# Kernel tuning notes

Hardware: AMD Instinct MI355X
Metric: run time of the kernel (lower is better)

The kernel has to match this reference:

```python
import jax, jax.numpy as jnp
import numpy as np

BN, BE, B = 50000, 800000, 16
NE, EE, GE, EH, NH = 32, 32, 32, 128, 128  # emb dims, hidden dims


def clean(x):
    return jnp.nan_to_num(x, nan=0.0, posinf=0.0, neginf=0.0)


def _lin(key, fan_in, fan_out):
    k1, k2 = jax.random.split(key)
    s = 1.0 / np.sqrt(fan_in)
    return (jax.random.uniform(k1, (fan_in, fan_out), jnp.float32, -s, s),
            jax.random.uniform(k2, (fan_out,), jnp.float32, -s, s))


def setup_inputs() -> dict:
    key = jax.random.key(0)
    ks = jax.random.split(key, 20)
    inp = {
        "x": jax.random.normal(ks[0], (BN, 2), jnp.float32),
        "edge_index": jax.random.randint(ks[1], (2, BE), 0, BN, jnp.int32),
        "batch": jax.random.randint(ks[2], (BN,), 0, B, jnp.int32),
        "node_attr": jnp.ones((BN, 2), jnp.float32),
        "edge_attr": jax.random.uniform(ks[3], (BE, 2), jnp.float32) + 0.5,  # positive spacings
        "glob_attr": jax.random.uniform(ks[4], (B, 2), jnp.float32),
    }
    # encoders (output 2*emb each, 'Duplicated')
    inp["enc_node_W"], inp["enc_node_b"] = _lin(ks[5], 2, 2 * NE)
    inp["enc_edge_W"], inp["enc_edge_b"] = _lin(ks[6], 2, 2 * EE)
    inp["enc_glob_W"], inp["enc_glob_b"] = _lin(ks[7], 2, 2 * GE)
    inp["enc2_W"], inp["enc2_b"] = _lin(ks[8], 2, 2 * EE)
    # derivative MLP: 4*NE+2*EE -> EH -> 2*EE
    inp["dW1"], inp["db1"] = _lin(ks[9], 4 * NE + 2 * EE, EH)
    inp["dW2"], inp["db2"] = _lin(ks[10], EH, 2 * EE)
    # half-jacobian MLP: 4*EE -> EH -> 2*EE
    inp["hW1"], inp["hb1"] = _lin(ks[11], 4 * EE, EH)
    inp["hW2"], inp["hb2"] = _lin(ks[12], EH, 2 * EE)
    # jacobian MLP: 6*EE -> NH -> 2*NE
    inp["jW1"], inp["jb1"] = _lin(ks[13], 6 * EE, NH)
    inp["jW2"], inp["jb2"] = _lin(ks[14], NH, 2 * NE)
    # hessian MLP: 4*EE+2*EE -> NH -> 2*NE
    inp["sW1"], inp["sb1"] = _lin(ks[15], 6 * EE, NH)
    inp["sW2"], inp["sb2"] = _lin(ks[16], NH, 2 * NE)
    # node MLP: 6*NE+2*GE -> NH -> 2*NE
    inp["nW1"], inp["nb1"] = _lin(ks[17], 6 * NE + 2 * GE, NH)
    inp["nW2"], inp["nb2"] = _lin(ks[18], NH, 2 * NE)
    # decoder: 2*NE -> 2
    inp["decW"], inp["decb"] = _lin(ks[19], 2 * NE, 2)
    return inp


def reference(x, edge_index, batch, node_attr, edge_attr, glob_attr,
              enc_node_W, enc_node_b, enc_edge_W, enc_edge_b, enc_glob_W, enc_glob_b,
              enc2_W, enc2_b,
              dW1, db1, dW2, db2,
              hW1, hb1, hW2, hb2,
              jW1, jb1, jW2, jb2,
              sW1, sb1, sW2, sb2,
              nW1, nb1, nW2, nb2,
              decW, decb):
    relu = jax.nn.relu
    seg = lambda d, idx: jax.ops.segment_sum(d, idx, num_segments=BN)
    mlp = lambda t, W1, b1, W2, b2: relu(t @ W1 + b1) @ W2 + b2

    row, col = edge_index[0], edge_index[1]
    spacing = edge_attr                                 # [BE,2]
    inv_spacing = clean(1.0 / spacing)
    inv_double = clean(1.0 / (seg(spacing, row) + seg(spacing, col)))  # [BN,2]

    node_emb = relu(x @ enc_node_W + enc_node_b)        # [BN,2*NE]
    spacing_emb = relu(spacing @ enc_edge_W + enc_edge_b)  # [BE,2*EE]
    glob_emb = relu(glob_attr @ enc_glob_W + enc_glob_b)   # [B,2*GE]
    inv_spacing_emb = relu(inv_spacing @ enc2_W + enc2_b)  # [BE,2*EE]
    inv_double_emb = relu(inv_double @ enc2_W + enc2_b)    # [BN,2*EE]

    d_edge = mlp(jnp.concatenate([node_emb[row], node_emb[col], inv_spacing_emb], -1),
                 dW1, db1, dW2, db2)                    # [BE,2*EE]
    hj_plus = seg(d_edge, row)                          # [BN,2*EE]
    hj_minus = seg(d_edge, col)

    jac1 = seg(mlp(jnp.concatenate([spacing_emb, hj_plus[col]], -1), hW1, hb1, hW2, hb2), col)
    jac2 = seg(mlp(jnp.concatenate([spacing_emb, hj_minus[row]], -1), hW1, hb1, hW2, hb2), row)
    jac = mlp(jnp.concatenate([jac1, jac2, inv_double_emb], -1), jW1, jb1, jW2, jb2)  # [BN,2*NE]

    hess = mlp(jnp.concatenate([hj_plus, hj_minus, inv_double_emb], -1), sW1, sb1, sW2, sb2)

    res = mlp(jnp.concatenate([node_emb, jac, glob_emb[batch], hess], -1), nW1, nb1, nW2, nb2)
    return node_attr * (res @ decW + decb)              # [BN,2]
```

## Files before the change

kernel.cpp:

```cpp
#include <hip/hip_runtime.h>
#include <hip/hip_fp16.h>
#include <math.h>

#define BN 50000
#define BE 800000
#define CHUNK 104
#define NWAVES 7693

typedef _Float16 h2 __attribute__((ext_vector_type(2)));

__device__ __forceinline__ float relu_f(float v) { return fmaxf(v, 0.0f); }
__device__ __forceinline__ float inv_clean(float s) {
    float q = 1.0f / s;
    return isfinite(q) ? q : 0.0f;
}
__device__ __forceinline__ float inv_clean_fast(float s) {
    float q = __builtin_amdgcn_rcpf(s);
    return isfinite(q) ? q : 0.0f;
}
__device__ __forceinline__ float fdot2f(h2 a, h2 b, float c) {
    return __builtin_amdgcn_fdot2(a, b, c, false);
}
__device__ __forceinline__ unsigned int h2u(h2 v) { union { h2 h; unsigned int u; } x; x.h = v; return x.u; }
__device__ __forceinline__ h2 uh2(unsigned int v) { union { unsigned int u; h2 h; } x; x.u = v; return x.h; }
__device__ __forceinline__ unsigned int packh2(float a, float b) {
    h2 h; h.x = (_Float16)a; h.y = (_Float16)b; return h2u(h);
}
__device__ __forceinline__ int pad4(int i) { return i + (i >> 3); }

__global__ __launch_bounds__(256) void k_pack_w1(
    const float* __restrict__ W, int r0, float4* __restrict__ dst)
{
    int t = blockIdx.x * 256 + threadIdx.x;
    if (t >= 2048) return;
    int j2 = t >> 6, l = t & 63;
    const float* ra = W + (size_t)(r0 + 2*j2) * 128 + 2*l;
    const float* rb = W + (size_t)(r0 + 2*j2 + 1) * 128 + 2*l;
    dst[t] = make_float4(ra[0], ra[1], rb[0], rb[1]);
}
__global__ __launch_bounds__(256) void k_pack_uv(
    const float* __restrict__ dW1, float4* __restrict__ dst)
{
    int t = blockIdx.x * 256 + threadIdx.x;
    if (t >= 4096) return;
    int j = t >> 6, l = t & 63;
    float4 w;
    if (l < 32) w = ((const float4*)(dW1 + (size_t)j*128))[l];
    else        w = ((const float4*)(dW1 + (size_t)(64+j)*128))[l-32];
    dst[t] = w;
}
__global__ __launch_bounds__(256) void k_pack_w1h(
    const float* __restrict__ W, int r0, uint2* __restrict__ dst)
{
    int t = blockIdx.x * 256 + threadIdx.x;
    if (t >= 2048) return;
    int j2 = t >> 6, l = t & 63;
    const float* ra = W + (size_t)(r0 + 2*j2) * 128;
    const float* rb = W + (size_t)(r0 + 2*j2 + 1) * 128;
    dst[t] = make_uint2(packh2(ra[2*l],   rb[2*l]),
                        packh2(ra[2*l+1], rb[2*l+1]));
}
__global__ __launch_bounds__(256) void k_pack_w2h(
    const float* __restrict__ W2, uint2* __restrict__ dst)
{
    int t = blockIdx.x * 256 + threadIdx.x;
    if (t >= 2048) return;
    int k4 = t >> 6, l = t & 63;
    dst[t] = make_uint2(packh2(W2[(4*k4+0)*64+l], W2[(4*k4+1)*64+l]),
                        packh2(W2[(4*k4+2)*64+l], W2[(4*k4+3)*64+l]));
}

__global__ __launch_bounds__(256) void k_hist(
    const int* __restrict__ ei, int* __restrict__ rc, int* __restrict__ cc)
{
    int e = blockIdx.x * 256 + threadIdx.x;
    if (e >= BE) return;
    atomicAdd(&rc[ei[e]], 1);
    atomicAdd(&cc[ei[BE + e]], 1);
}

__global__ __launch_bounds__(1024) void k_scan(
    const int* __restrict__ cntR, int* __restrict__ hdR,
    const int* __restrict__ cntC, int* __restrict__ hdC)
{
    __shared__ int s[1024];
    const int* cnt; int* hd;
    if (blockIdx.x == 0) { cnt = cntR; hd = hdR; }
    else                 { cnt = cntC; hd = hdC; }
    int t = threadIdx.x;
    int base = t * 49;
    int sum = 0;
    for (int i = 0; i < 49; i++) {
        int idx = base + i;
        sum += (idx < BN) ? cnt[idx] : 0;
    }
    s[t] = sum;
    __syncthreads();
    for (int o = 1; o < 1024; o <<= 1) {
        int v = (t >= o) ? s[t - o] : 0;
        __syncthreads();
        s[t] += v;
        __syncthreads();
    }
    int run = s[t] - sum;
    for (int i = 0; i < 49; i++) {
        int idx = base + i;
        if (idx < BN) { hd[idx] = run; run += cnt[idx]; }
    }
}

__global__ __launch_bounds__(256) void k_scatter2(
    const int* __restrict__ ei, const float* __restrict__ ea,
    int* __restrict__ rhd, int* __restrict__ chd,
    int4* __restrict__ rs, int4* __restrict__ cs)
{
    int e = blockIdx.x * 256 + threadIdx.x;
    if (e >= BE) return;
    int r = ei[e], c = ei[BE + e];
    float2 s = ((const float2*)ea)[e];
    int s0 = __float_as_int(s.x), s1 = __float_as_int(s.y);
    int p1 = atomicAdd(&rhd[r], 1);
    rs[p1] = make_int4(r, c, s0, s1);
// ... 66 lines not shown
        const int q = l >> 5;
        {
            float2 xa = ((const float2*)x)[n0 + q*4 + 0];
            float2 xb = ((const float2*)x)[n0 + q*4 + 1];
            float2 xc = ((const float2*)x)[n0 + q*4 + 2];
            float2 xd = ((const float2*)x)[n0 + q*4 + 3];
            float4 p0, p1;
            p0.x = relu_f(fmaf(xa.x, w0a, fmaf(xa.y, w0b, b0)));
            p0.y = relu_f(fmaf(xb.x, w0a, fmaf(xb.y, w0b, b0)));
            p0.z = relu_f(fmaf(xc.x, w0a, fmaf(xc.y, w0b, b0)));
            p0.w = relu_f(fmaf(xd.x, w0a, fmaf(xd.y, w0b, b0)));
            p1.x = relu_f(fmaf(xa.x, w1a, fmaf(xa.y, w1b, b1)));
            p1.y = relu_f(fmaf(xb.x, w1a, fmaf(xb.y, w1b, b1)));
            p1.z = relu_f(fmaf(xc.x, w1a, fmaf(xc.y, w1b, b1)));
            p1.w = relu_f(fmaf(xd.x, w1a, fmaf(xd.y, w1b, b1)));
            xb4[jj*2 + q]      = p0;
            xb4[(jj+32)*2 + q] = p1;
        }
        float4 acc[8];
        #pragma unroll
        for (int e = 0; e < 8; e++) acc[e] = make_float4(0,0,0,0);
        #pragma unroll 8
        for (int j = 0; j < 64; j++) {
            float4 wq = guv[j*64 + l];
            float4 xa = xb4[j*2 + 0];
            float4 xc = xb4[j*2 + 1];
            acc[0].x = fmaf(xa.x, wq.x, acc[0].x); acc[0].y = fmaf(xa.x, wq.y, acc[0].y);
            acc[0].z = fmaf(xa.x, wq.z, acc[0].z); acc[0].w = fmaf(xa.x, wq.w, acc[0].w);
            acc[1].x = fmaf(xa.y, wq.x, acc[1].x); acc[1].y = fmaf(xa.y, wq.y, acc[1].y);
            acc[1].z = fmaf(xa.y, wq.z, acc[1].z); acc[1].w = fmaf(xa.y, wq.w, acc[1].w);
            acc[2].x = fmaf(xa.z, wq.x, acc[2].x); acc[2].y = fmaf(xa.z, wq.y, acc[2].y);
            acc[2].z = fmaf(xa.z, wq.z, acc[2].z); acc[2].w = fmaf(xa.z, wq.w, acc[2].w);
            acc[3].x = fmaf(xa.w, wq.x, acc[3].x); acc[3].y = fmaf(xa.w, wq.y, acc[3].y);
            acc[3].z = fmaf(xa.w, wq.z, acc[3].z); acc[3].w = fmaf(xa.w, wq.w, acc[3].w);
            acc[4].x = fmaf(xc.x, wq.x, acc[4].x); acc[4].y = fmaf(xc.x, wq.y, acc[4].y);
            acc[4].z = fmaf(xc.x, wq.z, acc[4].z); acc[4].w = fmaf(xc.x, wq.w, acc[4].w);
            acc[5].x = fmaf(xc.y, wq.x, acc[5].x); acc[5].y = fmaf(xc.y, wq.y, acc[5].y);
            acc[5].z = fmaf(xc.y, wq.z, acc[5].z); acc[5].w = fmaf(xc.y, wq.w, acc[5].w);
            acc[6].x = fmaf(xc.z, wq.x, acc[6].x); acc[6].y = fmaf(xc.z, wq.y, acc[6].y);
            acc[6].z = fmaf(xc.z, wq.z, acc[6].z); acc[6].w = fmaf(xc.z, wq.w, acc[6].w);
            acc[7].x = fmaf(xc.w, wq.x, acc[7].x); acc[7].y = fmaf(xc.w, wq.y, acc[7].y);
            acc[7].z = fmaf(xc.w, wq.z, acc[7].z); acc[7].w = fmaf(xc.w, wq.w, acc[7].w);
        }
        __half* dst = (l < 32) ? (u_h + 4*l) : (v_h + 4*(l-32));
        #pragma unroll
        for (int e = 0; e < 8; e++) {
            __half2* p = (__half2*)(dst + (size_t)(n0+e)*128);
            p[0] = __floats2half2_rn(acc[e].x, acc[e].y);
            p[1] = __floats2half2_rn(acc[e].z, acc[e].w);
        }
    }
}

__global__ __launch_bounds__(256, 4) void k_e1(
    const int4* __restrict__ recs,
    const __half* __restrict__ A_h, const __half* __restrict__ B_h,
    const int* __restrict__ lb, const int* __restrict__ hd, const int* __restrict__ cnt,
    const float* __restrict__ e2w, const float* __restrict__ e2b,
    const uint2* __restrict__ pw1, const float* __restrict__ db1,
    const uint2* __restrict__ pw2, const float* __restrict__ db2,
    float* __restrict__ outAcc)
{
    extern __shared__ unsigned int ldsu[];
    const int wid = threadIdx.x >> 6, l = threadIdx.x & 63;
    uint4* xbuf = (uint4*)ldsu + (size_t)wid * 216;
    uint4* hbuf = xbuf + 72;

    const int wave = blockIdx.x * 4 + wid;
    if (wave >= NWAVES) return;
    const int n0 = lb[wave], n1 = lb[wave + 1];
    if (n0 >= n1) return;
    const int eb = hd[n0] - cnt[n0];
    const int ee = (n1 < BN) ? (hd[n1] - cnt[n1]) : BE;
    if (eb >= ee) return;

    const int j2 = l >> 1, eh = l & 1;
    const float w0a = e2w[2*j2],    w0b = e2w[64+2*j2], eb0 = e2b[2*j2];
    const float w1a = e2w[2*j2+1],  w1b = e2w[65+2*j2], eb1 = e2b[2*j2+1];
    const float b1a = db1[2*l], b1b = db1[2*l+1];
    const float b2r = db2[l];

    float acc = 0.f;
    int cur = -1;

    for (int i = eb; i < ee; i += 8) {
        const int nact = min(8, ee - i);
        int key[8], oth[8];
        float spx[8], spy[8];
        #pragma unroll
        for (int e = 0; e < 8; e++) {
            int idx = i + ((e < nact) ? e : nact - 1);
            int4 rec = recs[idx];
            key[e] = rec.x; oth[e] = rec.y;
            spx[e] = __int_as_float(rec.z); spy[e] = __int_as_float(rec.w);
        }
        {
            uint4 xw;
            unsigned int* xp = (unsigned int*)&xw;
            #pragma unroll
            for (int c = 0; c < 4; c++) {
                int e = 4*eh + c;
                float q0 = inv_clean_fast(spx[e]);
                float q1 = inv_clean_fast(spy[e]);
                float r0 = relu_f(fmaf(q0, w0a, fmaf(q1, w0b, eb0)));
                float r1 = relu_f(fmaf(q0, w1a, fmaf(q1, w1b, eb1)));
                xp[c] = packh2(r0, r1);
            }
            xbuf[pad4(j2*2 + eh)] = xw;
        }
        float t0[8], t1[8];
        #pragma unroll
        for (int e = 0; e < 8; e++) {
            float2 au = __half22float2(*(const __half2*)(A_h + (size_t)key[e]*128 + 2*l));
            float2 bu = __half22float2(*(const __half2*)(B_h + (size_t)oth[e]*128 + 2*l));
            t0[e] = b1a + au.x + bu.x;
            t1[e] = b1b + au.y + bu.y;
        }
        #pragma unroll 8
        for (int p = 0; p < 32; p++) {
            uint4 x0 = xbuf[pad4(p*2 + 0)];
            uint4 x1 = xbuf[pad4(p*2 + 1)];
            uint2 wv = pw1[p*64 + l];
            h2 wa = uh2(wv.x), wb = uh2(wv.y);
            t0[0] = fdot2f(uh2(x0.x), wa, t0[0]); t1[0] = fdot2f(uh2(x0.x), wb, t1[0]);
            t0[1] = fdot2f(uh2(x0.y), wa, t0[1]); t1[1] = fdot2f(uh2(x0.y), wb, t1[1]);
            t0[2] = fdot2f(uh2(x0.z), wa, t0[2]); t1[2] = fdot2f(uh2(x0.z), wb, t1[2]);
            t0[3] = fdot2f(uh2(x0.w), wa, t0[3]); t1[3] = fdot2f(uh2(x0.w), wb, t1[3]);
            t0[4] = fdot2f(uh2(x1.x), wa, t0[4]); t1[4] = fdot2f(uh2(x1.x), wb, t1[4]);
            t0[5] = fdot2f(uh2(x1.y), wa, t0[5]); t1[5] = fdot2f(uh2(x1.y), wb, t1[5]);
            t0[6] = fdot2f(uh2(x1.z), wa, t0[6]); t1[6] = fdot2f(uh2(x1.z), wb, t1[6]);
            t0[7] = fdot2f(uh2(x1.w), wa, t0[7]); t1[7] = fdot2f(uh2(x1.w), wb, t1[7]);
        }
        {
            uint4 hA, hB;
            unsigned int* pa = (unsigned int*)&hA;
            unsigned int* pb = (unsigned int*)&hB;
            #pragma unroll
            for (int c = 0; c < 4; c++) {
                pa[c] = packh2(relu_f(t0[c]),   relu_f(t1[c]));
                pb[c] = packh2(relu_f(t0[4+c]), relu_f(t1[4+c]));
            }
            hbuf[pad4(l*2 + 0)] = hA;
            hbuf[pad4(l*2 + 1)] = hB;
        }
        float o[8] = {0,0,0,0,0,0,0,0};
        #pragma unroll 8
        for (int k4 = 0; k4 < 32; k4++) {
            uint4 a0 = hbuf[pad4(4*k4 + 0)];
            uint4 a1 = hbuf[pad4(4*k4 + 1)];
            uint4 b0 = hbuf[pad4(4*k4 + 2)];
            uint4 b1 = hbuf[pad4(4*k4 + 3)];
            uint2 wv = pw2[k4*64 + l];
            h2 wa = uh2(wv.x), wb = uh2(wv.y);
            o[0] = fdot2f(uh2(b0.x), wb, fdot2f(uh2(a0.x), wa, o[0]));
            o[1] = fdot2f(uh2(b0.y), wb, fdot2f(uh2(a0.y), wa, o[1]));
            o[2] = fdot2f(uh2(b0.z), wb, fdot2f(uh2(a0.z), wa, o[2]));
            o[3] = fdot2f(uh2(b0.w), wb, fdot2f(uh2(a0.w), wa, o[3]));
            o[4] = fdot2f(uh2(b1.x), wb, fdot2f(uh2(a1.x), wa, o[4]));
            o[5] = fdot2f(uh2(b1.y), wb, fdot2f(uh2(a1.y), wa, o[5]));
            o[6] = fdot2f(uh2(b1.z), wb, fdot2f(uh2(a1.z), wa, o[6]));
            o[7] = fdot2f(uh2(b1.w), wb, fdot2f(uh2(a1.w), wa, o[7]));
        }
        #pragma unroll
        for (int e = 0; e < 8; e++) {
            if (e < nact) {
                float val = o[e] + b2r;
                if (key[e] != cur) {
                    if (cur >= 0) outAcc[(size_t)cur*64 + l] = acc;
                    acc = 0.f;
                    cur = key[e];
                }
                acc += val;
            }
        }
    }
    if (cur >= 0) outAcc[(size_t)cur*64 + l] = acc;
}

__global__ __launch_bounds__(256, 6) void k_tptmh(
    const float* __restrict__ hjp, const float* __restrict__ hjm,
    const float4* __restrict__ gtp,
    __half* __restrict__ tp_h, __half* __restrict__ tm_h)
{
    extern __shared__ float lds[];
    const int wid = threadIdx.x >> 6, l = threadIdx.x & 63;
    float4* xb4 = (float4*)(lds + wid * 512);
    const int gw = blockIdx.x * 4 + wid;
    const int nw = gridDim.x * 4;
    const int NG = BN/8;

    for (int vg = gw; vg < 2*NG; vg += nw) {
        const float* in = (vg < NG) ? hjp : hjm;
        __half*     out = (vg < NG) ? tp_h : tm_h;
        const int n0 = ((vg < NG) ? vg : vg - NG) * 8;
        const int q = l >> 5;
        #pragma unroll
        for (int r = 0; r < 2; r++) {
            int j = (l & 31) + 32*r;
            float v0 = in[(n0 + q*4 + 0)*64 + j];
            float v1 = in[(n0 + q*4 + 1)*64 + j];
            float v2 = in[(n0 + q*4 + 2)*64 + j];
            float v3 = in[(n0 + q*4 + 3)*64 + j];
            xb4[j*2 + q] = make_float4(v0, v1, v2, v3);
        }
        float a0[8] = {0,0,0,0,0,0,0,0}, a1[8] = {0,0,0,0,0,0,0,0};
        #pragma unroll 8
        for (int j2 = 0; j2 < 32; j2++) {
            float4 wq = gtp[j2*64 + l];
            float4 xa = xb4[(2*j2)*2 + 0];
            float4 xbv = xb4[(2*j2)*2 + 1];
            float4 xc = xb4[(2*j2+1)*2 + 0];
            float4 xd = xb4[(2*j2+1)*2 + 1];
            a0[0] = fmaf(xa.x, wq.x, fmaf(xc.x, wq.z, a0[0]));
            a1[0] = fmaf(xa.x, wq.y, fmaf(xc.x, wq.w, a1[0]));
            a0[1] = fmaf(xa.y, wq.x, fmaf(xc.y, wq.z, a0[1]));
            a1[1] = fmaf(xa.y, wq.y, fmaf(xc.y, wq.w, a1[1]));
            a0[2] = fmaf(xa.z, wq.x, fmaf(xc.z, wq.z, a0[2]));
            a1[2] = fmaf(xa.z, wq.y, fmaf(xc.z, wq.w, a1[2]));
            a0[3] = fmaf(xa.w, wq.x, fmaf(xc.w, wq.z, a0[3]));
            a1[3] = fmaf(xa.w, wq.y, fmaf(xc.w, wq.w, a1[3]));
            a0[4] = fmaf(xbv.x, wq.x, fmaf(xd.x, wq.z, a0[4]));
            a1[4] = fmaf(xbv.x, wq.y, fmaf(xd.x, wq.w, a1[4]));
            a0[5] = fmaf(xbv.y, wq.x, fmaf(xd.y, wq.z, a0[5]));
            a1[5] = fmaf(xbv.y, wq.y, fmaf(xd.y, wq.w, a1[5]));
            a0[6] = fmaf(xbv.z, wq.x, fmaf(xd.z, wq.z, a0[6]));
            a1[6] = fmaf(xbv.z, wq.y, fmaf(xd.z, wq.w, a1[6]));
            a0[7] = fmaf(xbv.w, wq.x, fmaf(xd.w, wq.z, a0[7]));
            a1[7] = fmaf(xbv.w, wq.y, fmaf(xd.w, wq.w, a1[7]));
        }
        #pragma unroll
        for (int e = 0; e < 8; e++) {
            *(__half2*)(out + (size_t)(n0+e)*128 + 2*l) = __floats2half2_rn(a0[e], a1[e]);
        }
    }
}

__global__ __launch_bounds__(256, 4) void k_e2(
    const int4* __restrict__ recs, const __half* __restrict__ tvals_h,
    const int* __restrict__ lb, const int* __restrict__ hd, const int* __restrict__ cnt,
    const float* __restrict__ eew, const float* __restrict__ eeb,
    const uint2* __restrict__ pw1, const float* __restrict__ hb1,
    const uint2* __restrict__ pw2, const float* __restrict__ hb2,
    float* __restrict__ out)
{
    extern __shared__ unsigned int ldsu[];
    const int wid = threadIdx.x >> 6, l = threadIdx.x & 63;
    uint4* xbuf = (uint4*)ldsu + (size_t)wid * 216;
    uint4* hbuf = xbuf + 72;

    const int wave = blockIdx.x * 4 + wid;
    if (wave >= NWAVES) return;
    const int n0 = lb[wave], n1 = lb[wave + 1];
    if (n0 >= n1) return;
    const int eb = hd[n0] - cnt[n0];
    const int ee = (n1 < BN) ? (hd[n1] - cnt[n1]) : BE;
    if (eb >= ee) return;

    const int j2 = l >> 1, eh = l & 1;
    const float w0a = eew[2*j2],    w0b = eew[64+2*j2], eb0 = eeb[2*j2];
    const float w1a = eew[2*j2+1],  w1b = eew[65+2*j2], eb1 = eeb[2*j2+1];
    const float b1a = hb1[2*l], b1b = hb1[2*l+1];
    const float b2r = hb2[l];

    float acc = 0.f;
    int cur = -1;

    for (int i = eb; i < ee; i += 8) {
        const int nact = min(8, ee - i);
        int key[8];
        float spx[8], spy[8];
        #pragma unroll
        for (int e = 0; e < 8; e++) {
            int idx = i + ((e < nact) ? e : nact - 1);
            int4 rec = recs[idx];
            key[e] = rec.x;
            spx[e] = __int_as_float(rec.z); spy[e] = __int_as_float(rec.w);
        }
        {
            uint4 xw;
            unsigned int* xp = (unsigned int*)&xw;
            #pragma unroll
            for (int c = 0; c < 4; c++) {
                int e = 4*eh + c;
                float r0 = relu_f(fmaf(spx[e], w0a, fmaf(spy[e], w0b, eb0)));
                float r1 = relu_f(fmaf(spx[e], w1a, fmaf(spy[e], w1b, eb1)));
                xp[c] = packh2(r0, r1);
            }
            xbuf[pad4(j2*2 + eh)] = xw;
        }
        float t0[8], t1[8];
        #pragma unroll
        for (int e = 0; e < 8; e++) {
            float2 tv = __half22float2(*(const __half2*)(tvals_h + (size_t)key[e]*128 + 2*l));
            t0[e] = b1a + tv.x;
            t1[e] = b1b + tv.y;
        }
        #pragma unroll 8
        for (int p = 0; p < 32; p++) {
            uint4 x0 = xbuf[pad4(p*2 + 0)];
            uint4 x1 = xbuf[pad4(p*2 + 1)];
            uint2 wv = pw1[p*64 + l];
            h2 wa = uh2(wv.x), wb = uh2(wv.y);
            t0[0] = fdot2f(uh2(x0.x), wa, t0[0]); t1[0] = fdot2f(uh2(x0.x), wb, t1[0]);
            t0[1] = fdot2f(uh2(x0.y), wa, t0[1]); t1[1] = fdot2f(uh2(x0.y), wb, t1[1]);
            t0[2] = fdot2f(uh2(x0.z), wa, t0[2]); t1[2] = fdot2f(uh2(x0.z), wb, t1[2]);
            t0[3] = fdot2f(uh2(x0.w), wa, t0[3]); t1[3] = fdot2f(uh2(x0.w), wb, t1[3]);
            t0[4] = fdot2f(uh2(x1.x), wa, t0[4]); t1[4] = fdot2f(uh2(x1.x), wb, t1[4]);
            t0[5] = fdot2f(uh2(x1.y), wa, t0[5]); t1[5] = fdot2f(uh2(x1.y), wb, t1[5]);
            t0[6] = fdot2f(uh2(x1.z), wa, t0[6]); t1[6] = fdot2f(uh2(x1.z), wb, t1[6]);
            t0[7] = fdot2f(uh2(x1.w), wa, t0[7]); t1[7] = fdot2f(uh2(x1.w), wb, t1[7]);
        }
        {
            uint4 hA, hB;
            unsigned int* pa = (unsigned int*)&hA;
            unsigned int* pb = (unsigned int*)&hB;
            #pragma unroll
            for (int c = 0; c < 4; c++) {
                pa[c] = packh2(relu_f(t0[c]),   relu_f(t1[c]));
                pb[c] = packh2(relu_f(t0[4+c]), relu_f(t1[4+c]));
            }
            hbuf[pad4(l*2 + 0)] = hA;
            hbuf[pad4(l*2 + 1)] = hB;
        }
        float o[8] = {0,0,0,0,0,0,0,0};
        #pragma unroll 8
        for (int k4 = 0; k4 < 32; k4++) {
            uint4 a0 = hbuf[pad4(4*k4 + 0)];
            uint4 a1 = hbuf[pad4(4*k4 + 1)];
            uint4 b0 = hbuf[pad4(4*k4 + 2)];
            uint4 b1 = hbuf[pad4(4*k4 + 3)];
            uint2 wv = pw2[k4*64 + l];
            h2 wa = uh2(wv.x), wb = uh2(wv.y);
            o[0] = fdot2f(uh2(b0.x), wb, fdot2f(uh2(a0.x), wa, o[0]));
            o[1] = fdot2f(uh2(b0.y), wb, fdot2f(uh2(a0.y), wa, o[1]));
            o[2] = fdot2f(uh2(b0.z), wb, fdot2f(uh2(a0.z), wa, o[2]));
            o[3] = fdot2f(uh2(b0.w), wb, fdot2f(uh2(a0.w), wa, o[3]));
            o[4] = fdot2f(uh2(b1.x), wb, fdot2f(uh2(a1.x), wa, o[4]));
            o[5] = fdot2f(uh2(b1.y), wb, fdot2f(uh2(a1.y), wa, o[5]));
            o[6] = fdot2f(uh2(b1.z), wb, fdot2f(uh2(a1.z), wa, o[6]));
            o[7] = fdot2f(uh2(b1.w), wb, fdot2f(uh2(a1.w), wa, o[7]));
        }
        #pragma unroll
        for (int e = 0; e < 8; e++) {
            if (e < nact) {
                float val = o[e] + b2r;
                if (key[e] != cur) {
                    if (cur >= 0) out[(size_t)cur*64 + l] = acc;
                    acc = 0.f;
                    cur = key[e];
                }
                acc += val;
            }
        }
    }
    if (cur >= 0) out[(size_t)cur*64 + l] = acc;
}

__global__ __launch_bounds__(256, 4) void k_node_mlp(
    const float* __restrict__ A, const float* __restrict__ Bv,
    const float* __restrict__ sumsp,
    const float* __restrict__ e2w_g, const float* __restrict__ e2b_g,
    const float* __restrict__ W1g, const float* __restrict__ b1g,
    const float* __restrict__ W2g, const float* __restrict__ b2g,
    float* __restrict__ outp)
{
    extern __shared__ float lds[];
    const int wid = threadIdx.x >> 6, l = threadIdx.x & 63;
    float* xbuf = lds + wid * 768;
    float* hbuf = lds + 4*768 + wid * 512;

    const float ewl = e2w_g[l], ewl2 = e2w_g[64+l], ebl = e2b_g[l];
    const float bb0 = b1g[2*l], bb1 = b1g[2*l+1];
    const float bo = b2g[l];

    const int gw = blockIdx.x * 4 + wid;
    const int nw = gridDim.x * 4;

    for (int g = gw; g < BN/4; g += nw) {
        const int i0 = g * 4;
        float av[4], bv[4], iv[4];
        #pragma unroll
        for (int e = 0; e < 4; e++) {
            int i = i0 + e;
            av[e] = A[i*64 + l];
            bv[e] = Bv[i*64 + l];
            float q0 = inv_clean(sumsp[i*2+0]);
            float q1 = inv_clean(sumsp[i*2+1]);
            iv[e] = relu_f(fmaf(q0, ewl, fmaf(q1, ewl2, ebl)));
        }
        ((float4*)xbuf)[l]       = make_float4(av[0], av[1], av[2], av[3]);
        ((float4*)xbuf)[64 + l]  = make_float4(bv[0], bv[1], bv[2], bv[3]);
        ((float4*)xbuf)[128 + l] = make_float4(iv[0], iv[1], iv[2], iv[3]);

        float acc0[4] = {0,0,0,0}, acc1[4] = {0,0,0,0};
        #pragma unroll 8
        for (int j = 0; j < 192; j++) {
            float4 xv = ((const float4*)xbuf)[j];
            float2 wv = ((const float2*)(W1g + j*128))[l];
            acc0[0] = fmaf(xv.x, wv.x, acc0[0]);
            acc0[1] = fmaf(xv.y, wv.x, acc0[1]);
            acc0[2] = fmaf(xv.z, wv.x, acc0[2]);
            acc0[3] = fmaf(xv.w, wv.x, acc0[3]);
            acc1[0] = fmaf(xv.x, wv.y, acc1[0]);
            acc1[1] = fmaf(xv.y, wv.y, acc1[1]);
            acc1[2] = fmaf(xv.z, wv.y, acc1[2]);
            acc1[3] = fmaf(xv.w, wv.y, acc1[3]);
        }
        #pragma unroll
// ... 101 lines not shown
        }
    }
}

extern "C" void kernel_launch(void* const* d_in, const int* in_sizes, int n_in,
                              void* d_out, int out_size, void* d_ws, size_t ws_size,
                              hipStream_t stream) {
    const float* x          = (const float*)d_in[0];
    const int*   ei         = (const int*)  d_in[1];
    const int*   batch      = (const int*)  d_in[2];
    const float* node_attr  = (const float*)d_in[3];
    const float* edge_attr  = (const float*)d_in[4];
    const float* glob_attr  = (const float*)d_in[5];
    const float* enc_node_W = (const float*)d_in[6];
    const float* enc_node_b = (const float*)d_in[7];
    const float* enc_edge_W = (const float*)d_in[8];
    const float* enc_edge_b = (const float*)d_in[9];
    const float* enc_glob_W = (const float*)d_in[10];
    const float* enc_glob_b = (const float*)d_in[11];
    const float* enc2_W     = (const float*)d_in[12];
    const float* enc2_b     = (const float*)d_in[13];
    const float* dW1 = (const float*)d_in[14]; const float* db1 = (const float*)d_in[15];
    const float* dW2 = (const float*)d_in[16]; const float* db2 = (const float*)d_in[17];
    const float* hW1 = (const float*)d_in[18]; const float* hb1 = (const float*)d_in[19];
    const float* hW2 = (const float*)d_in[20]; const float* hb2 = (const float*)d_in[21];
    const float* jW1 = (const float*)d_in[22]; const float* jb1 = (const float*)d_in[23];
    const float* jW2 = (const float*)d_in[24]; const float* jb2 = (const float*)d_in[25];
    const float* sW1 = (const float*)d_in[26]; const float* sb1 = (const float*)d_in[27];
    const float* sW2 = (const float*)d_in[28]; const float* sb2 = (const float*)d_in[29];
    const float* nW1 = (const float*)d_in[30]; const float* nb1 = (const float*)d_in[31];
    const float* nW2 = (const float*)d_in[32]; const float* nb2 = (const float*)d_in[33];
    const float* decW = (const float*)d_in[34]; const float* decb = (const float*)d_in[35];

    float* ws = (float*)d_ws;
    int4*   rs    = (int4*)ws;
    int4*   cs    = (int4*)(ws + 3200000);
    __half* u_h   = (__half*)(ws + 6400000);
    __half* v_h   = (__half*)(ws + 9600000);
    float*  hjp   = ws + 12800000;
    float*  hjm   = ws + 16000000;
    float*  jac1  = ws + 19200000;
    float*  jac2  = ws + 22400000;
    float*  sumsp = ws + 25600000;
    int*    row_cnt = (int*)(ws + 25700000);
    int*    col_cnt = row_cnt + 50176;
    int*    row_hd  = col_cnt + 50176;
    int*    col_hd  = row_hd + 50048;
    int*    lbr     = col_hd + 50048;
    int*    lbc     = lbr + 7694;

    float* scratch = (float*)d_out;
    float4* puv   = (float4*)(scratch);
    float4* ptp   = (float4*)(scratch + 16384);
    uint2*  pe1w1 = (uint2*)(scratch + 24576);
    uint2*  pe1w2 = (uint2*)(scratch + 28672);
    uint2*  pe2w1 = (uint2*)(scratch + 32768);
    uint2*  pe2w2 = (uint2*)(scratch + 36864);

    hipMemsetAsync(hjp, 0, (size_t)12800000*sizeof(float), stream);
    hipMemsetAsync(row_cnt, 0, (size_t)(2*50176)*sizeof(int), stream);

    k_pack_uv<<<16, 256, 0, stream>>>(dW1, puv);
    k_pack_w1<<<8, 256, 0, stream>>>(hW1, 64, ptp);
    k_pack_w1h<<<8, 256, 0, stream>>>(dW1, 128, pe1w1);
    k_pack_w2h<<<8, 256, 0, stream>>>(dW2, pe1w2);
    k_pack_w1h<<<8, 256, 0, stream>>>(hW1, 0, pe2w1);
    k_pack_w2h<<<8, 256, 0, stream>>>(hW2, pe2w2);

    k_uvh<<<1563, 256, 2048*4, stream>>>(x, enc_node_W, enc_node_b, puv, u_h, v_h);

    k_hist<<<3125, 256, 0, stream>>>(ei, row_cnt, col_cnt);
    k_scan<<<2, 1024, 0, stream>>>(row_cnt, row_hd, col_cnt, col_hd);
    k_scatter2<<<3125, 256, 0, stream>>>(ei, edge_attr, row_hd, col_hd, rs, cs);
    k_sumsp2<<<196, 256, 0, stream>>>(rs, row_hd, row_cnt, cs, col_hd, col_cnt, sumsp);
    k_part<<<61, 256, 0, stream>>>(row_hd, row_cnt, lbr, col_hd, col_cnt, lbc);

    const int E_BLOCKS = (NWAVES + 3) / 4;
    const size_t lds_e = 4 * 216 * 16;

    k_e1<<<E_BLOCKS, 256, lds_e, stream>>>(rs, u_h, v_h, lbr, row_hd, row_cnt,
                                           enc2_W, enc2_b, pe1w1, db1, pe1w2, db2, hjp);
    k_e1<<<E_BLOCKS, 256, lds_e, stream>>>(cs, v_h, u_h, lbc, col_hd, col_cnt,
                                           enc2_W, enc2_b, pe1w1, db1, pe1w2, db2, hjm);

    k_tptmh<<<1536, 256, 2048*4, stream>>>(hjp, hjm, ptp, u_h, v_h);

    k_e2<<<E_BLOCKS, 256, lds_e, stream>>>(cs, u_h, lbc, col_hd, col_cnt,
                                           enc_edge_W, enc_edge_b,
                                           pe2w1, hb1, pe2w2, hb2, jac1);
    k_e2<<<E_BLOCKS, 256, lds_e, stream>>>(rs, v_h, lbr, row_hd, row_cnt,
                                           enc_edge_W, enc_edge_b,
                                           pe2w1, hb1, pe2w2, hb2, jac2);

    size_t lds_nm = (4*768 + 4*512) * sizeof(float);
    k_node_mlp<<<1024, 256, lds_nm, stream>>>(jac1, jac2, sumsp, enc2_W, enc2_b,
                                              jW1, jb1, jW2, jb2, jac1);
    k_node_mlp<<<1024, 256, lds_nm, stream>>>(hjp, hjm, sumsp, enc2_W, enc2_b,
                                              sW1, sb1, sW2, sb2, hjp);

    size_t lds_nf = (4*1024 + 4*512) * sizeof(float);
    k_node_final<<<1024, 256, lds_nf, stream>>>(x, enc_node_W, enc_node_b,
                                                jac1, hjp,
                                                batch, glob_attr, enc_glob_W, enc_glob_b,
                                                nW1, nb1, nW2, nb2, decW, decb,
                                                node_attr, (float*)d_out);
}
```

Baseline: 2.416 ms.

## Replace fdot2 edge-MLP kernels with MFMA 16x16x16 fp16 templated kernel

Rewrites the two per-edge MLP kernels (derivative and half-jacobian) into one templated kernel that processes 16 edges per wave using MFMA 16x16x16 fp16 instructions instead of scalar fdot2 loops through LDS. Weights are repacked into MFMA fragment layout, and the first-layer inputs are built directly in registers. The second-layer output goes through a small LDS tile for the segmented row reduction. This aims to cut the VALU-bound dot-product cost on the 800k-edge passes, at the cost of more per-lane gather granularity and new fragment-layout correctness risk.

After: 2.409 ms. No clear change (-0.3%).

```diff
diff --git a/kernel.cpp b/kernel.cpp
--- a/kernel.cpp
+++ b/kernel.cpp
@@ -8,6 +8,8 @@
 #define NWAVES 7693
 
 typedef _Float16 h2 __attribute__((ext_vector_type(2)));
+typedef _Float16 h4 __attribute__((ext_vector_type(4)));
+typedef float    f4 __attribute__((ext_vector_type(4)));
 
 __device__ __forceinline__ float relu_f(float v) { return fmaxf(v, 0.0f); }
 __device__ __forceinline__ float inv_clean(float s) {
@@ -18,15 +20,12 @@
     float q = __builtin_amdgcn_rcpf(s);
     return isfinite(q) ? q : 0.0f;
 }
-__device__ __forceinline__ float fdot2f(h2 a, h2 b, float c) {
-    return __builtin_amdgcn_fdot2(a, b, c, false);
-}
 __device__ __forceinline__ unsigned int h2u(h2 v) { union { h2 h; unsigned int u; } x; x.h = v; return x.u; }
 __device__ __forceinline__ h2 uh2(unsigned int v) { union { unsigned int u; h2 h; } x; x.u = v; return x.h; }
 __device__ __forceinline__ unsigned int packh2(float a, float b) {
     h2 h; h.x = (_Float16)a; h.y = (_Float16)b; return h2u(h);
 }
-__device__ __forceinline__ int pad4(int i) { return i + (i >> 3); }
+__device__ __forceinline__ h4 u2h4(uint2 v) { union { uint2 u; h4 h; } x; x.u = v; return x.h; }
 
 __global__ __launch_bounds__(256) void k_pack_w1(
     const float* __restrict__ W, int r0, float4* __restrict__ dst)
@@ -49,25 +48,35 @@
     else        w = ((const float4*)(dW1 + (size_t)(64+j)*128))[l-32];
     dst[t] = w;
 }
-__global__ __launch_bounds__(256) void k_pack_w1h(
+__global__ __launch_bounds__(256) void k_pack_a1(
     const float* __restrict__ W, int r0, uint2* __restrict__ dst)
 {
     int t = blockIdx.x * 256 + threadIdx.x;
     if (t >= 2048) return;
-    int j2 = t >> 6, l = t & 63;
-    const float* ra = W + (size_t)(r0 + 2*j2) * 128;
-    const float* rb = W + (size_t)(r0 + 2*j2 + 1) * 128;
-    dst[t] = make_uint2(packh2(ra[2*l],   rb[2*l]),
-                        packh2(ra[2*l+1], rb[2*l+1]));
-}
-__global__ __launch_bounds__(256) void k_pack_w2h(
+    int frag = t >> 6, l = t & 63;
+    int n = frag >> 2, s = frag & 3;
+    int i = l & 15, kq = l >> 4;
+    size_t base = (size_t)(r0 + s*16 + kq*4) * 128 + n*16 + i;
+    float w0 = W[base + 0*128];
+    float w1 = W[base + 1*128];
+    float w2 = W[base + 2*128];
+    float w3 = W[base + 3*128];
+    dst[t] = make_uint2(packh2(w0, w1), packh2(w2, w3));
+}
+__global__ __launch_bounds__(256) void k_pack_a2(
     const float* __restrict__ W2, uint2* __restrict__ dst)
 {
     int t = blockIdx.x * 256 + threadIdx.x;
     if (t >= 2048) return;
-    int k4 = t >> 6, l = t & 63;
-    dst[t] = make_uint2(packh2(W2[(4*k4+0)*64+l], W2[(4*k4+1)*64+l]),
-                        packh2(W2[(4*k4+2)*64+l], W2[(4*k4+3)*64+l]));
+    int frag = t >> 6, l = t & 63;
+    int m = frag >> 3, n = frag & 7;
+    int i = l & 15, kq = l >> 4;
+    size_t base = (size_t)(n*16 + kq*4) * 64 + m*16 + i;
+    float w0 = W2[base + 0*64];
+    float w1 = W2[base + 1*64];
+    float w2 = W2[base + 2*64];
+    float w3 = W2[base + 3*64];
+    dst[t] = make_uint2(packh2(w0, w1), packh2(w2, w3));
 }
 
 __global__ __launch_bounds__(256) void k_hist(
@@ -240,129 +249,115 @@
     }
 }
 
-__global__ __launch_bounds__(256, 4) void k_e1(
+template<int MODE>
+__global__ __launch_bounds__(256, 4) void k_em(
     const int4* __restrict__ recs,
     const __half* __restrict__ A_h, const __half* __restrict__ B_h,
     const int* __restrict__ lb, const int* __restrict__ hd, const int* __restrict__ cnt,
-    const float* __restrict__ e2w, const float* __restrict__ e2b,
-    const uint2* __restrict__ pw1, const float* __restrict__ db1,
-    const uint2* __restrict__ pw2, const float* __restrict__ db2,
-    float* __restrict__ outAcc)
-{
-    extern __shared__ unsigned int ldsu[];
-    const int wid = threadIdx.x >> 6, l = threadIdx.x & 63;
-    uint4* xbuf = (uint4*)ldsu + (size_t)wid * 216;
-    uint4* hbuf = xbuf + 72;
+    const float* __restrict__ ew, const float* __restrict__ ebv,
+    const uint2* __restrict__ pa1, const float* __restrict__ b1g,
+    const uint2* __restrict__ pa2, const float* __restrict__ b2g,
+    float* __restrict__ out)
+{
+    extern __shared__ float lds[];
+    const int l = threadIdx.x & 63, wid = threadIdx.x >> 6;
+    float* sbuf = lds + wid * (16 * 68);
 
     const int wave = blockIdx.x * 4 + wid;
     if (wave >= NWAVES) return;
-    const int n0 = lb[wave], n1 = lb[wave + 1];
-    if (n0 >= n1) return;
-    const int eb = hd[n0] - cnt[n0];
-    const int ee = (n1 < BN) ? (hd[n1] - cnt[n1]) : BE;
+    const int nlo = lb[wave], nhi = lb[wave + 1];
+    if (nlo >= nhi) return;
+    const int eb = hd[nlo] - cnt[nlo];
+    const int ee = (nhi < BN) ? (hd[nhi] - cnt[nhi]) : BE;
     if (eb >= ee) return;
 
-    const int j2 = l >> 1, eh = l & 1;
-    const float w0a = e2w[2*j2],    w0b = e2w[64+2*j2], eb0 = e2b[2*j2];
-    const float w1a = e2w[2*j2+1],  w1b = e2w[65+2*j2], eb1 = e2b[2*j2+1];
-    const float b1a = db1[2*l], b1b = db1[2*l+1];
-    const float b2r = db2[l];
+    const int kq = l >> 4, li = l & 15;
+    const float b2r = b2g[l];
 
     float acc = 0.f;
     int cur = -1;
 
-    for (int i = eb; i < ee; i += 8) {
-        const int nact = min(8, ee - i);
-        int key[8], oth[8];
-        float spx[8], spy[8];
-        #pragma unroll
-        for (int e = 0; e < 8; e++) {
-            int idx = i + ((e < nact) ? e : nact - 1);
-            int4 rec = recs[idx];
-            key[e] = rec.x; oth[e] = rec.y;
-            spx[e] = __int_as_float(rec.z); spy[e] = __int_as_float(rec.w);
-        }
-        {
-            uint4 xw;
-            unsigned int* xp = (unsigned int*)&xw;
+    for (int i0 = eb; i0 < ee; i0 += 16) {
+        const int nact = min(16, ee - i0);
+        int4 rec = recs[i0 + min(li, nact - 1)];
+        const int mykey = rec.x, myoth = rec.y;
+        float q0 = __int_as_float(rec.z), q1 = __int_as_float(rec.w);
+        if (MODE == 0) { q0 = inv_clean_fast(q0); q1 = inv_clean_fast(q1); }
+
+        h4 xb[4];
+        #pragma unroll
+        for (int s = 0; s < 4; s++) {
+            const float4 wA = *(const float4*)(ew + s*16 + kq*4);
+            const float4 wB = *(const float4*)(ew + 64 + s*16 + kq*4);
+            const float4 bb = *(const float4*)(ebv + s*16 + kq*4);
+            h4 xv;
+            xv[0] = (_Float16)relu_f(fmaf(q0, wA.x, fmaf(q1, wB.x, bb.x)));
+            xv[1] = (_Float16)relu_f(fmaf(q0, wA.y, fmaf(q1, wB.y, bb.y)));
+            xv[2] = (_Float16)relu_f(fmaf(q0, wA.z, fmaf(q1, wB.z, bb.z)));
+            xv[3] = (_Float16)relu_f(fmaf(q0, wA.w, fmaf(q1, wB.w, bb.w)));
+            xb[s] = xv;
+        }
+
+        h4 hf[8];
+        #pragma unroll
+        for (int n = 0; n < 8; n++) {
+            f4 a1 = {0.f, 0.f, 0.f, 0.f};
             #pragma unroll
-            for (int c = 0; c < 4; c++) {
-                int e = 4*eh + c;
-                float q0 = inv_clean_fast(spx[e]);
-                float q1 = inv_clean_fast(spy[e]);
-                float r0 = relu_f(fmaf(q0, w0a, fmaf(q1, w0b, eb0)));
-                float r1 = relu_f(fmaf(q0, w1a, fmaf(q1, w1b, eb1)));
-                xp[c] = packh2(r0, r1);
+            for (int s = 0; s < 4; s++)
+                a1 = __builtin_amdgcn_mfma_f32_16x16x16f16(
+                        u2h4(pa1[(n*4 + s)*64 + l]), xb[s], a1, 0, 0, 0);
+            const float4 b1q = *(const float4*)(b1g + n*16 + kq*4);
+            float t0, t1, t2, t3;
+            if (MODE == 0) {
+                uint2 uu = *(const uint2*)(A_h + (size_t)mykey*128 + n*16 + kq*4);
+                uint2 vv = *(const uint2*)(B_h + (size_t)myoth*128 + n*16 + kq*4);
+                h2 ul = uh2(uu.x), uhh = uh2(uu.y), vl = uh2(vv.x), vhh = uh2(vv.y);
+                t0 = a1[0] + b1q.x + (float)ul.x  + (float)vl.x;
+                t1 = a1[1] + b1q.y + (float)ul.y  + (float)vl.y;
+                t2 = a1[2] + b1q.z + (float)uhh.x + (float)vhh.x;
+                t3 = a1[3] + b1q.w + (float)uhh.y + (float)vhh.y;
+            } else {
+                uint2 tt = *(const uint2*)(A_h + (size_t)mykey*128 + n*16 + kq*4);
+                h2 tl = uh2(tt.x), th = uh2(tt.y);
+                t0 = a1[0] + b1q.x + (float)tl.x;
+                t1 = a1[1] + b1q.y + (float)tl.y;
+                t2 = a1[2] + b1q.z + (float)th.x;
+                t3 = a1[3] + b1q.w + (float)th.y;
             }
-            xbuf[pad4(j2*2 + eh)] = xw;
-        }
-        float t0[8], t1[8];
-        #pragma unroll
-        for (int e = 0; e < 8; e++) {
-            float2 au = __half22float2(*(const __half2*)(A_h + (size_t)key[e]*128 + 2*l));
-            float2 bu = __half22float2(*(const __half2*)(B_h + (size_t)oth[e]*128 + 2*l));
-            t0[e] = b1a + au.x + bu.x;
-            t1[e] = b1b + au.y + bu.y;
-        }
-        #pragma unroll 8
-        for (int p = 0; p < 32; p++) {
-            uint4 x0 = xbuf[pad4(p*2 + 0)];
-            uint4 x1 = xbuf[pad4(p*2 + 1)];
-            uint2 wv = pw1[p*64 + l];
-            h2 wa = uh2(wv.x), wb = uh2(wv.y);
-            t0[0] = fdot2f(uh2(x0.x), wa, t0[0]); t1[0] = fdot2f(uh2(x0.x), wb, t1[0]);
-            t0[1] = fdot2f(uh2(x0.y), wa, t0[1]); t1[1] = fdot2f(uh2(x0.y), wb, t1[1]);
-            t0[2] = fdot2f(uh2(x0.z), wa, t0[2]); t1[2] = fdot2f(uh2(x0.z), wb, t1[2]);
-            t0[3] = fdot2f(uh2(x0.w), wa, t0[3]); t1[3] = fdot2f(uh2(x0.w), wb, t1[3]);
-            t0[4] = fdot2f(uh2(x1.x), wa, t0[4]); t1[4] = fdot2f(uh2(x1.x), wb, t1[4]);
-            t0[5] = fdot2f(uh2(x1.y), wa, t0[5]); t1[5] = fdot2f(uh2(x1.y), wb, t1[5]);
-            t0[6] = fdot2f(uh2(x1.z), wa, t0[6]); t1[6] = fdot2f(uh2(x1.z), wb, t1[6]);
-            t0[7] = fdot2f(uh2(x1.w), wa, t0[7]); t1[7] = fdot2f(uh2(x1.w), wb, t1[7]);
-        }
-        {
-            uint4 hA, hB;
-            unsigned int* pa = (unsigned int*)&hA;
-            unsigned int* pb = (unsigned int*)&hB;
+            h4 hv;
+            hv[0] = (_Float16)relu_f(t0);
+            hv[1] = (_Float16)relu_f(t1);
+            hv[2] = (_Float16)relu_f(t2);
+            hv[3] = (_Float16)relu_f(t3);
+            hf[n] = hv;
+        }
+
+        #pragma unroll
+        for (int m = 0; m < 4; m++) {
+            f4 a2 = {0.f, 0.f, 0.f, 0.f};
             #pragma unroll
-            for (int c = 0; c < 4; c++) {
-                pa[c] = packh2(relu_f(t0[c]),   relu_f(t1[c]));
-                pb[c] = packh2(relu_f(t0[4+c]), relu_f(t1[4+c]));
-            }
-            hbuf[pad4(l*2 + 0)] = hA;
-            hbuf[pad4(l*2 + 1)] = hB;
-        }
-        float o[8] = {0,0,0,0,0,0,0,0};
-        #pragma unroll 8
-        for (int k4 = 0; k4 < 32; k4++) {
-            uint4 a0 = hbuf[pad4(4*k4 + 0)];
-            uint4 a1 = hbuf[pad4(4*k4 + 1)];
-            uint4 b0 = hbuf[pad4(4*k4 + 2)];
-            uint4 b1 = hbuf[pad4(4*k4 + 3)];
-            uint2 wv = pw2[k4*64 + l];
-            h2 wa = uh2(wv.x), wb = uh2(wv.y);
-            o[0] = fdot2f(uh2(b0.x), wb, fdot2f(uh2(a0.x), wa, o[0]));
-            o[1] = fdot2f(uh2(b0.y), wb, fdot2f(uh2(a0.y), wa, o[1]));
-            o[2] = fdot2f(uh2(b0.z), wb, fdot2f(uh2(a0.z), wa, o[2]));
-            o[3] = fdot2f(uh2(b0.w), wb, fdot2f(uh2(a0.w), wa, o[3]));
-            o[4] = fdot2f(uh2(b1.x), wb, fdot2f(uh2(a1.x), wa, o[4]));
-            o[5] = fdot2f(uh2(b1.y), wb, fdot2f(uh2(a1.y), wa, o[5]));
-            o[6] = fdot2f(uh2(b1.z), wb, fdot2f(uh2(a1.z), wa, o[6]));
-            o[7] = fdot2f(uh2(b1.w), wb, fdot2f(uh2(a1.w), wa, o[7]));
-        }
-        #pragma unroll
-        for (int e = 0; e < 8; e++) {
+            for (int n = 0; n < 8; n++)
+                a2 = __builtin_amdgcn_mfma_f32_16x16x16f16(
+                        u2h4(pa2[(m*8 + n)*64 + l]), hf[n], a2, 0, 0, 0);
+            *(float4*)(sbuf + li*68 + m*16 + kq*4) =
+                make_float4(a2[0], a2[1], a2[2], a2[3]);
+        }
+
+        #pragma unroll
+        for (int e = 0; e < 16; e++) {
             if (e < nact) {
-                float val = o[e] + b2r;
-                if (key[e] != cur) {
-                    if (cur >= 0) outAcc[(size_t)cur*64 + l] = acc;
+                int ke = __builtin_amdgcn_readlane(mykey, e);
+                float val = sbuf[e*68 + l] + b2r;
+                if (ke != cur) {
+                    if (cur >= 0) out[(size_t)cur*64 + l] = acc;
                     acc = 0.f;
-                    cur = key[e];
+                    cur = ke;
                 }
                 acc += val;
             }
         }
     }
-    if (cur >= 0) outAcc[(size_t)cur*64 + l] = acc;
+    if (cur >= 0) out[(size_t)cur*64 + l] = acc;
 }
 
 __global__ __launch_bounds__(256, 6) void k_tptmh(
@@ -421,127 +416,6 @@
             *(__half2*)(out + (size_t)(n0+e)*128 + 2*l) = __floats2half2_rn(a0[e], a1[e]);
         }
     }
-}
-
-__global__ __launch_bounds__(256, 4) void k_e2(
-    const int4* __restrict__ recs, const __half* __restrict__ tvals_h,
-    const int* __restrict__ lb, const int* __restrict__ hd, const int* __restrict__ cnt,
-    const float* __restrict__ eew, const float* __restrict__ eeb,
-    const uint2* __restrict__ pw1, const float* __restrict__ hb1,
-    const uint2* __restrict__ pw2, const float* __restrict__ hb2,
-    float* __restrict__ out)
-{
-    extern __shared__ unsigned int ldsu[];
-    const int wid = threadIdx.x >> 6, l = threadIdx.x & 63;
-    uint4* xbuf = (uint4*)ldsu + (size_t)wid * 216;
-    uint4* hbuf = xbuf + 72;
-
-    const int wave = blockIdx.x * 4 + wid;
-    if (wave >= NWAVES) return;
-    const int n0 = lb[wave], n1 = lb[wave + 1];
-    if (n0 >= n1) return;
-    const int eb = hd[n0] - cnt[n0];
-    const int ee = (n1 < BN) ? (hd[n1] - cnt[n1]) : BE;
-    if (eb >= ee) return;
-
-    const int j2 = l >> 1, eh = l & 1;
-    const float w0a = eew[2*j2],    w0b = eew[64+2*j2], eb0 = eeb[2*j2];
-    const float w1a = eew[2*j2+1],  w1b = eew[65+2*j2], eb1 = eeb[2*j2+1];
-    const float b1a = hb1[2*l], b1b = hb1[2*l+1];
-    const float b2r = hb2[l];
-
-    float acc = 0.f;
-    int cur = -1;
-
-    for (int i = eb; i < ee; i += 8) {
-        const int nact = min(8, ee - i);
-        int key[8];
-        float spx[8], spy[8];
-        #pragma unroll
-        for (int e = 0; e < 8; e++) {
-            int idx = i + ((e < nact) ? e : nact - 1);
-            int4 rec = recs[idx];
-            key[e] = rec.x;
-            spx[e] = __int_as_float(rec.z); spy[e] = __int_as_float(rec.w);
-        }
-        {
-            uint4 xw;
-            unsigned int* xp = (unsigned int*)&xw;
-            #pragma unroll
-            for (int c = 0; c < 4; c++) {
-                int e = 4*eh + c;
-                float r0 = relu_f(fmaf(spx[e], w0a, fmaf(spy[e], w0b, eb0)));
-                float r1 = relu_f(fmaf(spx[e], w1a, fmaf(spy[e], w1b, eb1)));
-                xp[c] = packh2(r0, r1);
-            }
-            xbuf[pad4(j2*2 + eh)] = xw;
-        }
-        float t0[8], t1[8];
-        #pragma unroll
-        for (int e = 0; e < 8; e++) {
-            float2 tv = __half22float2(*(const __half2*)(tvals_h + (size_t)key[e]*128 + 2*l));
-            t0[e] = b1a + tv.x;
-            t1[e] = b1b + tv.y;
-        }
-        #pragma unroll 8
-        for (int p = 0; p < 32; p++) {
-            uint4 x0 = xbuf[pad4(p*2 + 0)];
-            uint4 x1 = xbuf[pad4(p*2 + 1)];
-            uint2 wv = pw1[p*64 + l];
-            h2 wa = uh2(wv.x), wb = uh2(wv.y);
-            t0[0] = fdot2f(uh2(x0.x), wa, t0[0]); t1[0] = fdot2f(uh2(x0.x), wb, t1[0]);
-            t0[1] = fdot2f(uh2(x0.y), wa, t0[1]); t1[1] = fdot2f(uh2(x0.y), wb, t1[1]);
-            t0[2] = fdot2f(uh2(x0.z), wa, t0[2]); t1[2] = fdot2f(uh2(x0.z), wb, t1[2]);
-            t0[3] = fdot2f(uh2(x0.w), wa, t0[3]); t1[3] = fdot2f(uh2(x0.w), wb, t1[3]);
-            t0[4] = fdot2f(uh2(x1.x), wa, t0[4]); t1[4] = fdot2f(uh2(x1.x), wb, t1[4]);
-            t0[5] = fdot2f(uh2(x1.y), wa, t0[5]); t1[5] = fdot2f(uh2(x1.y), wb, t1[5]);
-            t0[6] = fdot2f(uh2(x1.z), wa, t0[6]); t1[6] = fdot2f(uh2(x1.z), wb, t1[6]);
-            t0[7] = fdot2f(uh2(x1.w), wa, t0[7]); t1[7] = fdot2f(uh2(x1.w), wb, t1[7]);
-        }
-        {
-            uint4 hA, hB;
-            unsigned int* pa = (unsigned int*)&hA;
-            unsigned int* pb = (unsigned int*)&hB;
-            #pragma unroll
-            for (int c = 0; c < 4; c++) {
-                pa[c] = packh2(relu_f(t0[c]),   relu_f(t1[c]));
-                pb[c] = packh2(relu_f(t0[4+c]), relu_f(t1[4+c]));
-            }
-            hbuf[pad4(l*2 + 0)] = hA;
-            hbuf[pad4(l*2 + 1)] = hB;
-        }
-        float o[8] = {0,0,0,0,0,0,0,0};
-        #pragma unroll 8
-        for (int k4 = 0; k4 < 32; k4++) {
-            uint4 a0 = hbuf[pad4(4*k4 + 0)];
-            uint4 a1 = hbuf[pad4(4*k4 + 1)];
-            uint4 b0 = hbuf[pad4(4*k4 + 2)];
-            uint4 b1 = hbuf[pad4(4*k4 + 3)];
-            uint2 wv = pw2[k4*64 + l];
-            h2 wa = uh2(wv.x), wb = uh2(wv.y);
-            o[0] = fdot2f(uh2(b0.x), wb, fdot2f(uh2(a0.x), wa, o[0]));
-            o[1] = fdot2f(uh2(b0.y), wb, fdot2f(uh2(a0.y), wa, o[1]));
-            o[2] = fdot2f(uh2(b0.z), wb, fdot2f(uh2(a0.z), wa, o[2]));
-            o[3] = fdot2f(uh2(b0.w), wb, fdot2f(uh2(a0.w), wa, o[3]));
-            o[4] = fdot2f(uh2(b1.x), wb, fdot2f(uh2(a1.x), wa, o[4]));
-            o[5] = fdot2f(uh2(b1.y), wb, fdot2f(uh2(a1.y), wa, o[5]));
-            o[6] = fdot2f(uh2(b1.z), wb, fdot2f(uh2(a1.z), wa, o[6]));
-            o[7] = fdot2f(uh2(b1.w), wb, fdot2f(uh2(a1.w), wa, o[7]));
-        }
-        #pragma unroll
-        for (int e = 0; e < 8; e++) {
-            if (e < nact) {
-                float val = o[e] + b2r;
-                if (key[e] != cur) {
-                    if (cur >= 0) out[(size_t)cur*64 + l] = acc;
-                    acc = 0.f;
-                    cur = key[e];
-                }
-                acc += val;
-            }
-        }
-    }
-    if (cur >= 0) out[(size_t)cur*64 + l] = acc;
 }
 
 __global__ __launch_bounds__(256, 4) void k_node_mlp(
@@ -749,20 +623,20 @@
     float* scratch = (float*)d_out;
     float4* puv   = (float4*)(scratch);
     float4* ptp   = (float4*)(scratch + 16384);
-    uint2*  pe1w1 = (uint2*)(scratch + 24576);
-    uint2*  pe1w2 = (uint2*)(scratch + 28672);
-    uint2*  pe2w1 = (uint2*)(scratch + 32768);
-    uint2*  pe2w2 = (uint2*)(scratch + 36864);
+    uint2*  pa1e1 = (uint2*)(scratch + 24576);
+    uint2*  pa2e1 = (uint2*)(scratch + 28672);
+    uint2*  pa1e2 = (uint2*)(scratch + 32768);
+    uint2*  pa2e2 = (uint2*)(scratch + 36864);
 
     hipMemsetAsync(hjp, 0, (size_t)12800000*sizeof(float), stream);
     hipMemsetAsync(row_cnt, 0, (size_t)(2*50176)*sizeof(int), stream);
 
     k_pack_uv<<<16, 256, 0, stream>>>(dW1, puv);
     k_pack_w1<<<8, 256, 0, stream>>>(hW1, 64, ptp);
-    k_pack_w1h<<<8, 256, 0, stream>>>(dW1, 128, pe1w1);
-    k_pack_w2h<<<8, 256, 0, stream>>>(dW2, pe1w2);
-    k_pack_w1h<<<8, 256, 0, stream>>>(hW1, 0, pe2w1);
-    k_pack_w2h<<<8, 256, 0, stream>>>(hW2, pe2w2);
+    k_pack_a1<<<8, 256, 0, stream>>>(dW1, 128, pa1e1);
+    k_pack_a2<<<8, 256, 0, stream>>>(dW2, pa2e1);
+    k_pack_a1<<<8, 256, 0, stream>>>(hW1, 0, pa1e2);
+    k_pack_a2<<<8, 256, 0, stream>>>(hW2, pa2e2);
 
     k_uvh<<<1563, 256, 2048*4, stream>>>(x, enc_node_W, enc_node_b, puv, u_h, v_h);
 
@@ -773,21 +647,19 @@
     k_part<<<61, 256, 0, stream>>>(row_hd, row_cnt, lbr, col_hd, col_cnt, lbc);
 
     const int E_BLOCKS = (NWAVES + 3) / 4;
-    const size_t lds_e = 4 * 216 * 16;
-
-    k_e1<<<E_BLOCKS, 256, lds_e, stream>>>(rs, u_h, v_h, lbr, row_hd, row_cnt,
-                                           enc2_W, enc2_b, pe1w1, db1, pe1w2, db2, hjp);
-    k_e1<<<E_BLOCKS, 256, lds_e, stream>>>(cs, v_h, u_h, lbc, col_hd, col_cnt,
-                                           enc2_W, enc2_b, pe1w1, db1, pe1w2, db2, hjm);
+    const size_t lds_e = 4 * 16 * 68 * sizeof(float);
+
+    k_em<0><<<E_BLOCKS, 256, lds_e, stream>>>(rs, u_h, v_h, lbr, row_hd, row_cnt,
+                                              enc2_W, enc2_b, pa1e1, db1, pa2e1, db2, hjp);
+    k_em<0><<<E_BLOCKS, 256, lds_e, stream>>>(cs, v_h, u_h, lbc, col_hd, col_cnt,
+                                              enc2_W, enc2_b, pa1e1, db1, pa2e1, db2, hjm);
 
     k_tptmh<<<1536, 256, 2048*4, stream>>>(hjp, hjm, ptp, u_h, v_h);
 
-    k_e2<<<E_BLOCKS, 256, lds_e, stream>>>(cs, u_h, lbc, col_hd, col_cnt,
-                                           enc_edge_W, enc_edge_b,
-                                           pe2w1, hb1, pe2w2, hb2, jac1);
-    k_e2<<<E_BLOCKS, 256, lds_e, stream>>>(rs, v_h, lbr, row_hd, row_cnt,
-                                           enc_edge_W, enc_edge_b,
-                                           pe2w1, hb1, pe2w2, hb2, jac2);
+    k_em<1><<<E_BLOCKS, 256, lds_e, stream>>>(cs, u_h, u_h, lbc, col_hd, col_cnt,
+                                              enc_edge_W, enc_edge_b, pa1e2, hb1, pa2e2, hb2, jac1);
+    k_em<1><<<E_BLOCKS, 256, lds_e, stream>>>(rs, v_h, v_h, lbr, row_hd, row_cnt,
+                                              enc_edge_W, enc_edge_b, pa1e2, hb1, pa2e2, hb2, jac2);
 
     size_t lds_nm = (4*768 + 4*512) * sizeof(float);
     k_node_mlp<<<1024, 256, lds_nm, stream>>>(jac1, jac2, sumsp, enc2_W, enc2_b,
```
